# Optimization experiments

Measured on AMD Instinct MI355X. Metric: run time of the kernel, lower is better.

## Reference

```python
import jax, jax.numpy as jnp
import numpy as np

B, N, K = 4, 4096, 16
EPS = 1e-12


def setup_inputs() -> dict:
    key = jax.random.key(0)
    k1, k2, k3 = jax.random.split(key, 3)
    ori = jax.random.normal(k1, (B, N, 3), dtype=jnp.float32)
    # adversarial cloud = original + small perturbation (realistic attack setting)
    adv = ori + 0.05 * jax.random.normal(k2, (B, N, 3), dtype=jnp.float32)
    nrm = jax.random.normal(k3, (B, N, 3), dtype=jnp.float32)
    nrm = nrm / (jnp.linalg.norm(nrm, axis=-1, keepdims=True) + EPS)  # unit normals
    return {"ori_pcs": ori, "adv_pcs": adv, "ori_normals": nrm, "k": K}


def _sqdist(a, b):
    # a: [B,N,3], b: [B,M,3] -> [B,N,M] squared euclidean distances (GEMM form)
    return ((a * a).sum(-1)[:, :, None] + (b * b).sum(-1)[:, None, :]
            - 2.0 * jnp.einsum('bnd,bmd->bnm', a, b))


def _gather_rows(pts, idx):
    # pts: [B,M,3], idx: [B,...] int -> [B,...,3]
    return jax.vmap(lambda p, i: p[i])(pts, idx)


def _kappa(pc, normals, k):
    # curvature proxy: mean |<normalized offset to kNN, normal>| per point -> [B,N]
    d = _sqdist(pc, pc)                       # [B,N,N]
    _, idx = jax.lax.top_k(-d, k + 1)         # nearest k+1 (incl. self)
    idx = idx[..., 1:]                        # drop self -> [B,N,k]
    nn = _gather_rows(pc, idx)                # [B,N,k,3]
    vec = nn - pc[:, :, None, :]
    vec = vec / (jnp.linalg.norm(vec, axis=-1, keepdims=True) + EPS)
    return jnp.abs(jnp.einsum('bnkd,bnd->bnk', vec, normals)).mean(-1)


def reference(ori_pcs, adv_pcs, ori_normals, k):
    # curvature of the clean cloud
    kappa_ori = _kappa(ori_pcs, ori_normals, k)            # [B,N]
    # adv points borrow the normal of their nearest original point
    d = _sqdist(adv_pcs, ori_pcs)                          # [B,N,N]
    nn_idx = jnp.argmin(d, axis=-1)                        # [B,N]
    adv_normals = _gather_rows(ori_normals, nn_idx)        # [B,N,3]
    kappa_adv = _kappa(adv_pcs, adv_normals, k)            # [B,N]
    # std of curvature over points (torch.std -> unbiased, ddof=1)
    std_ori = jnp.std(kappa_ori, axis=1, ddof=1)           # [B]
    std_adv = jnp.std(kappa_adv, axis=1, ddof=1)           # [B]
    return jnp.mean(jnp.abs(std_adv - std_ori))
```

## Files before the change

kernel.cpp:

```cpp
#include <hip/hip_runtime.h>
#include <math.h>

#define B_ 4
#define N_ 4096
#define K_ 16
#define NT 64
#define INF __builtin_huge_valf()
#define SLACK 1e-3f

__device__ __forceinline__ float dpp_shr1_f(float x) {
    return __int_as_float(__builtin_amdgcn_update_dpp(
        __float_as_int(x), __float_as_int(x), 0x111, 0xF, 0xF, false));
}
__device__ __forceinline__ int dpp_shr1_i(int x) {
    return __builtin_amdgcn_update_dpp(x, x, 0x111, 0xF, 0xF, false);
}
__device__ __forceinline__ float readlane_f(float x, int l) {
    return __int_as_float(__builtin_amdgcn_readlane(__float_as_int(x), l));
}
__device__ __forceinline__ float rflf(float x) {
    return __int_as_float(__builtin_amdgcn_readfirstlane(__float_as_int(x)));
}
#if __has_builtin(__builtin_amdgcn_inverse_ballot_w64)
#define LANEBIT(m, lane) __builtin_amdgcn_inverse_ballot_w64(m)
#else
#define LANEBIT(m, lane) ((((m) >> (lane)) & 1ull) != 0)
#endif

#define POP1(mi, di, sdi, sii, tb)                                         \
    {   int src = __builtin_ctzll(mi); mi &= mi - 1;                       \
        float v = readlane_f(di, src);                                     \
        int  vi = (tb) + src;                                              \
        unsigned long long mg = __ballot(sdi > v);                         \
        float usd = dpp_shr1_f(sdi); int usi = dpp_shr1_i(sii);            \
        bool gt = LANEBIT(mg, lane);                                       \
        bool pg = LANEBIT(mg << 1, lane);                                  \
        sdi = gt ? (pg ? usd : v ) : sdi;                                  \
        sii = gt ? (pg ? usi : vi) : sii; }

__device__ __forceinline__ int spread4(int v) {
    return (v & 1) | ((v & 2) << 2) | ((v & 4) << 4) | ((v & 8) << 6);
}

__device__ __forceinline__ float aabb2f(float4 lo, float4 hi,
                                        float qx, float qy, float qz) {
    float dx = fmaxf(fmaxf(lo.x - qx, qx - hi.x), 0.f);
    float dy = fmaxf(fmaxf(lo.y - qy, qy - hi.y), 0.f);
    float dz = fmaxf(fmaxf(lo.z - qz, qz - hi.z), 0.f);
    return fmaf(dz, dz, fmaf(dy, dy, dx*dx));
}

#define TILE_SORT(sk, st)                                                  \
    _Pragma("unroll")                                                      \
    for (int k = 2; k <= 64; k <<= 1) {                                    \
        _Pragma("unroll")                                                  \
        for (int jj = k >> 1; jj > 0; jj >>= 1) {                          \
            bool sel = ((lane & k) == 0) == ((lane & jj) == 0);            \
            float o = __shfl_xor(sk, jj); int a2 = __shfl_xor(st, jj);     \
            bool oless = (o < sk) || (o == sk && a2 < st);                 \
            if (oless == sel) { sk = o; st = a2; }                         \
        }                                                                  \
    }

__global__ __launch_bounds__(1024) void morton_sort_kernel(
    const float* __restrict__ ori, const float* __restrict__ adv,
    float4* __restrict__ gs, int* __restrict__ gidx)
{
    __shared__ int hist[4096];
    __shared__ int wsum[1024];
    const int tid = threadIdx.x;
    const int set = blockIdx.x >> 2, b = blockIdx.x & 3;
    const float* src = (set ? adv : ori) + (size_t)b * (N_*3);
    float4* dst = gs + (size_t)blockIdx.x * N_;
    int*    dsi = gidx + (size_t)blockIdx.x * N_;

    #pragma unroll
    for (int k = 0; k < 4; ++k) hist[k*1024 + tid] = 0;
    __syncthreads();

    float px[4], py[4], pz[4]; int code[4];
    #pragma unroll
    for (int k = 0; k < 4; ++k) {
        int j = k*1024 + tid;
        float x = src[3*j+0], y = src[3*j+1], z = src[3*j+2];
        px[k] = x; py[k] = y; pz[k] = z;
        int ix = (int)((x + 4.25f) * (16.0f/8.5f));
        int iy = (int)((y + 4.25f) * (16.0f/8.5f));
        int iz = (int)((z + 4.25f) * (16.0f/8.5f));
        ix = ix < 0 ? 0 : (ix > 15 ? 15 : ix);
        iy = iy < 0 ? 0 : (iy > 15 ? 15 : iy);
        iz = iz < 0 ? 0 : (iz > 15 ? 15 : iz);
        code[k] = (spread4(ix) << 2) | (spread4(iy) << 1) | spread4(iz);
        atomicAdd(&hist[code[k]], 1);
    }
    __syncthreads();
    const int h0 = hist[4*tid], h1 = hist[4*tid+1],
              h2 = hist[4*tid+2], h3 = hist[4*tid+3];
    const int s = h0 + h1 + h2 + h3;
    wsum[tid] = s;
    __syncthreads();
    for (int st = 1; st < 1024; st <<= 1) {
        int tmp = (tid >= st) ? wsum[tid - st] : 0;
        __syncthreads();
        wsum[tid] += tmp;
        __syncthreads();
    }
    int eb = wsum[tid] - s;
    hist[4*tid]   = eb;
    hist[4*tid+1] = eb + h0;
    hist[4*tid+2] = eb + h0 + h1;
    hist[4*tid+3] = eb + h0 + h1 + h2;
    __syncthreads();
    #pragma unroll
    for (int k = 0; k < 4; ++k) {
        int j = k*1024 + tid;
        int pos = atomicAdd(&hist[code[k]], 1);
        float pp = fmaf(pz[k],pz[k], fmaf(py[k],py[k], px[k]*px[k]));
        dst[pos] = make_float4(px[k], py[k], pz[k], pp);
        dsi[pos] = j;
    }
}

__global__ __launch_bounds__(1024) void aabb_kernel(
    const float4* __restrict__ gs, float4* __restrict__ ab)
{
    const int tid = threadIdx.x, lane = tid & 63, w = tid >> 6;
    const float4* g = gs + (size_t)blockIdx.x * N_;
    float4* a = ab + (size_t)blockIdx.x * (NT*2);
    #pragma unroll
    for (int i = 0; i < 4; ++i) {
        int t = w*4 + i;
        float4 p = g[t*64 + lane];
        float x0=p.x, x1=p.x, y0=p.y, y1=p.y, z0=p.z, z1=p.z;
        #pragma unroll
        for (int s2 = 1; s2 < 64; s2 <<= 1) {
            x0 = fminf(x0, __shfl_xor(x0, s2)); x1 = fmaxf(x1, __shfl_xor(x1, s2));
            y0 = fminf(y0, __shfl_xor(y0, s2)); y1 = fmaxf(y1, __shfl_xor(y1, s2));
            z0 = fminf(z0, __shfl_xor(z0, s2)); z1 = fmaxf(z1, __shfl_xor(z1, s2));
        }
        if (lane == 0) {
            a[t*2+0] = make_float4(x0, y0, z0, 0.f);
            a[t*2+1] = make_float4(x1, y1, z1, 0.f);
        }
    }
}

__global__ __launch_bounds__(256) void curv_argmin_kernel(
    const float4* __restrict__ gs, const int* __restrict__ gidx,
    const float4* __restrict__ ab, int* __restrict__ nnidx)
{
    const int tid = threadIdx.x, lane = tid & 63;
    const int gw = blockIdx.x*4 + (tid >> 6);
    const int b  = gw >> 10;
    const int sq0 = (gw & 1023) * 4;
    const float4* go = gs + (size_t)b * N_;
    const int*    io = gidx + (size_t)b * N_;
    const float4* ga = gs + (size_t)(4+b) * N_;
    const int*    ia = gidx + (size_t)(4+b) * N_;
    const float4* abo = ab + (size_t)b * (NT*2);

    float4 f0 = ga[sq0+0], f1 = ga[sq0+1], f2 = ga[sq0+2], f3 = ga[sq0+3];
    const float q0x=rflf(f0.x), q0y=rflf(f0.y), q0z=rflf(f0.z), qq0=rflf(f0.w);
    const float q1x=rflf(f1.x), q1y=rflf(f1.y), q1z=rflf(f1.z), qq1=rflf(f1.w);
    const float q2x=rflf(f2.x), q2y=rflf(f2.y), q2z=rflf(f2.z), qq2=rflf(f2.w);
    const float q3x=rflf(f3.x), q3y=rflf(f3.y), q3z=rflf(f3.z), qq3=rflf(f3.w);
    const float m2x0=-2.f*q0x, m2y0=-2.f*q0y, m2z0=-2.f*q0z;
    const float m2x1=-2.f*q1x, m2y1=-2.f*q1y, m2z1=-2.f*q1z;
    const float m2x2=-2.f*q2x, m2y2=-2.f*q2y, m2z2=-2.f*q2z;
    const float m2x3=-2.f*q3x, m2y3=-2.f*q3y, m2z3=-2.f*q3z;

    float4 lo = abo[lane*2+0], hi = abo[lane*2+1];
    float sk = fminf(fminf(aabb2f(lo,hi,q0x,q0y,q0z), aabb2f(lo,hi,q1x,q1y,q1z)),
                     fminf(aabb2f(lo,hi,q2x,q2y,q2z), aabb2f(lo,hi,q3x,q3y,q3z)));
    int st = lane;
    TILE_SORT(sk, st)

    float dm0=INF,dm1=INF,dm2=INF,dm3=INF; int jm0=0,jm1=0,jm2=0,jm3=0;
    float bound = INF;
    for (int it = 0; it < NT; ++it) {
        float kd = readlane_f(sk, it);
        if (kd >= bound) break;
        int t = __builtin_amdgcn_readlane(st, it);
        int j = t*64 + lane;
        float4 p = go[j];
        float r0 = fmaf(p.z,m2z0, fmaf(p.y,m2y0, fmaf(p.x,m2x0, p.w)));
        float r1 = fmaf(p.z,m2z1, fmaf(p.y,m2y1, fmaf(p.x,m2x1, p.w)));
        float r2 = fmaf(p.z,m2z2, fmaf(p.y,m2y2, fmaf(p.x,m2x2, p.w)));
        float r3 = fmaf(p.z,m2z3, fmaf(p.y,m2y3, fmaf(p.x,m2x3, p.w)));
        if (r0 < dm0) { dm0 = r0; jm0 = j; }
        if (r1 < dm1) { dm1 = r1; jm1 = j; }
        if (r2 < dm2) { dm2 = r2; jm2 = j; }
        if (r3 < dm3) { dm3 = r3; jm3 = j; }
        float g0=dm0, g1=dm1, g2=dm2, g3=dm3;
        #pragma unroll
        for (int s2 = 1; s2 < 64; s2 <<= 1) {
            g0 = fminf(g0, __shfl_xor(g0, s2));
            g1 = fminf(g1, __shfl_xor(g1, s2));
            g2 = fminf(g2, __shfl_xor(g2, s2));
            g3 = fminf(g3, __shfl_xor(g3, s2));
        }
        bound = fmaxf(fmaxf(g0+qq0, g1+qq1), fmaxf(g2+qq2, g3+qq3)) + SLACK;
    }
    #pragma unroll
    for (int s2 = 1; s2 < 64; s2 <<= 1) {
        { float od=__shfl_xor(dm0,s2); int oj=__shfl_xor(jm0,s2);
          if (od<dm0 || (od==dm0 && oj<jm0)) { dm0=od; jm0=oj; } }
        { float od=__shfl_xor(dm1,s2); int oj=__shfl_xor(jm1,s2);
          if (od<dm1 || (od==dm1 && oj<jm1)) { dm1=od; jm1=oj; } }
        { float od=__shfl_xor(dm2,s2); int oj=__shfl_xor(jm2,s2);
          if (od<dm2 || (od==dm2 && oj<jm2)) { dm2=od; jm2=oj; } }
        { float od=__shfl_xor(dm3,s2); int oj=__shfl_xor(jm3,s2);
          if (od<dm3 || (od==dm3 && oj<jm3)) { dm3=od; jm3=oj; } }
    }
    if (lane == 0) {
        nnidx[b*N_ + ia[sq0+0]] = io[jm0];
        nnidx[b*N_ + ia[sq0+1]] = io[jm1];
        nnidx[b*N_ + ia[sq0+2]] = io[jm2];
        nnidx[b*N_ + ia[sq0+3]] = io[jm3];
    }
}

__global__ __launch_bounds__(256) void curv_kappa_kernel(
    const float4* __restrict__ gs, const int* __restrict__ gidx,
    const float4* __restrict__ ab, const float* __restrict__ nrm,
    const int* __restrict__ nnidx, double* __restrict__ acc)
{
    __shared__ double rs[4], rss[4];
    const int tid = threadIdx.x, lane = tid & 63, w = tid >> 6;
    const int gw = blockIdx.x*4 + w;
    const int job = gw >> 12;
    const int b   = (gw >> 10) & 3;
    const int sq0 = (gw & 1023) * 4;
    const float4* g  = gs + (size_t)(job*4+b) * N_;
    const int*    gi = gidx + (size_t)(job*4+b) * N_;
    const float4* abo = ab + (size_t)(job*4+b) * (NT*2);
    const float*  nb = nrm + (size_t)b * (N_*3);

    const int T0 = sq0 >> 6, sl = sq0 & 63;
    float4 f0 = g[sq0+0], f1 = g[sq0+1], f2 = g[sq0+2], f3 = g[sq0+3];
    const float q0x=rflf(f0.x), q0y=rflf(f0.y), q0z=rflf(f0.z), qq0=rflf(f0.w);
    const float q1x=rflf(f1.x), q1y=rflf(f1.y), q1z=rflf(f1.z), qq1=rflf(f1.w);
    const float q2x=rflf(f2.x), q2y=rflf(f2.y), q2z=rflf(f2.z), qq2=rflf(f2.w);
    const float q3x=rflf(f3.x), q3y=rflf(f3.y), q3z=rflf(f3.z), qq3=rflf(f3.w);
    const float m2x0=-2.f*q0x, m2y0=-2.f*q0y, m2z0=-2.f*q0z;
    const float m2x1=-2.f*q1x, m2y1=-2.f*q1y, m2z1=-2.f*q1z;
    const float m2x2=-2.f*q2x, m2y2=-2.f*q2y, m2z2=-2.f*q2z;
    const float m2x3=-2.f*q3x, m2y3=-2.f*q3y, m2z3=-2.f*q3z;

    const int n0 = __builtin_amdgcn_readfirstlane(gi[sq0+0]);
    const int n1 = __builtin_amdgcn_readfirstlane(gi[sq0+1]);
    const int n2 = __builtin_amdgcn_readfirstlane(gi[sq0+2]);
    const int n3 = __builtin_amdgcn_readfirstlane(gi[sq0+3]);
    const int nn0 = job ? nnidx[b*N_ + n0] : n0;
    const int nn1 = job ? nnidx[b*N_ + n1] : n1;
    const int nn2 = job ? nnidx[b*N_ + n2] : n2;
    const int nn3 = job ? nnidx[b*N_ + n3] : n3;
    const float nx0=rflf(nb[3*nn0+0]), ny0=rflf(nb[3*nn0+1]), nz0=rflf(nb[3*nn0+2]);
    const float nx1=rflf(nb[3*nn1+0]), ny1=rflf(nb[3*nn1+1]), nz1=rflf(nb[3*nn1+2]);
    const float nx2=rflf(nb[3*nn2+0]), ny2=rflf(nb[3*nn2+1]), nz2=rflf(nb[3*nn2+2]);
    const float nx3=rflf(nb[3*nn3+0]), ny3=rflf(nb[3*nn3+1]), nz3=rflf(nb[3*nn3+2]);

    float4 lo = abo[lane*2+0], hi = abo[lane*2+1];
    float sk = fminf(fminf(aabb2f(lo,hi,q0x,q0y,q0z), aabb2f(lo,hi,q1x,q1y,q1z)),
                     fminf(aabb2f(lo,hi,q2x,q2y,q2z), aabb2f(lo,hi,q3x,q3y,q3z)));
    int st = lane;
    TILE_SORT(sk, st)

    const int j0 = T0*64 + lane;
    float sd0, sd1, sd2, sd3;
    int   si0 = j0, si1 = j0, si2 = j0, si3 = j0;
    {
        float4 p = g[j0];
        sd0 = fmaf(p.z,m2z0, fmaf(p.y,m2y0, fmaf(p.x,m2x0, p.w)));
        sd1 = fmaf(p.z,m2z1, fmaf(p.y,m2y1, fmaf(p.x,m2x1, p.w)));
        sd2 = fmaf(p.z,m2z2, fmaf(p.y,m2y2, fmaf(p.x,m2x2, p.w)));
        sd3 = fmaf(p.z,m2z3, fmaf(p.y,m2y3, fmaf(p.x,m2x3, p.w)));
        if (lane == sl    ) sd0 = INF;
        if (lane == sl + 1) sd1 = INF;
        if (lane == sl + 2) sd2 = INF;
        if (lane == sl + 3) sd3 = INF;
    }
    #pragma unroll
    for (int k = 2; k <= 64; k <<= 1) {
        #pragma unroll
        for (int jj = k >> 1; jj > 0; jj >>= 1) {
            bool sel = ((lane & k) == 0) == ((lane & jj) == 0);
            { float o=__shfl_xor(sd0,jj); int a=__shfl_xor(si0,jj);
              if ((o<sd0)==sel) { sd0=o; si0=a; } }
            { float o=__shfl_xor(sd1,jj); int a=__shfl_xor(si1,jj);
              if ((o<sd1)==sel) { sd1=o; si1=a; } }
            { float o=__shfl_xor(sd2,jj); int a=__shfl_xor(si2,jj);
              if ((o<sd2)==sel) { sd2=o; si2=a; } }
            { float o=__shfl_xor(sd3,jj); int a=__shfl_xor(si3,jj);
              if ((o<sd3)==sel) { sd3=o; si3=a; } }
        }
    }
    float tau0 = readlane_f(sd0, 15), tau1 = readlane_f(sd1, 15);
    float tau2 = readlane_f(sd2, 15), tau3 = readlane_f(sd3, 15);
    float bound = fmaxf(fmaxf(tau0+qq0, tau1+qq1),
                        fmaxf(tau2+qq2, tau3+qq3)) + SLACK;

    for (int it = 0; it < NT; ++it) {
        float kd = readlane_f(sk, it);
        if (kd >= bound) break;
        int t = __builtin_amdgcn_readlane(st, it);
        if (t == T0) continue;
        int tb = t*64, j = tb + lane;
        float4 p = g[j];
        float d0 = fmaf(p.z,m2z0, fmaf(p.y,m2y0, fmaf(p.x,m2x0, p.w)));
        float d1 = fmaf(p.z,m2z1, fmaf(p.y,m2y1, fmaf(p.x,m2x1, p.w)));
        float d2 = fmaf(p.z,m2z2, fmaf(p.y,m2y2, fmaf(p.x,m2x2, p.w)));
        float d3 = fmaf(p.z,m2z3, fmaf(p.y,m2y3, fmaf(p.x,m2x3, p.w)));
        unsigned long long m0 = __ballot(d0 < tau0);
        unsigned long long m1 = __ballot(d1 < tau1);
        unsigned long long m2 = __ballot(d2 < tau2);
        unsigned long long m3 = __ballot(d3 < tau3);
        if (m0 | m1 | m2 | m3) {
            while (m0 | m1 | m2 | m3) {
                if (m0) POP1(m0, d0, sd0, si0, tb)
                if (m1) POP1(m1, d1, sd1, si1, tb)
                if (m2) POP1(m2, d2, sd2, si2, tb)
                if (m3) POP1(m3, d3, sd3, si3, tb)
            }
            tau0 = readlane_f(sd0, 15); tau1 = readlane_f(sd1, 15);
            tau2 = readlane_f(sd2, 15); tau3 = readlane_f(sd3, 15);
            bound = fmaxf(fmaxf(tau0+qq0, tau1+qq1),
                          fmaxf(tau2+qq2, tau3+qq3)) + SLACK;
        }
    }

    double ksum = 0.0, kss = 0.0;
#define KTAIL(siN, qxN, qyN, qzN, nxN, nyN, nzN)                           \
    {   float tl = 0.0f;                                                   \
        if (lane < K_) {                                                   \
            float4 p2 = g[siN];                                            \
            float vx = p2.x - qxN, vy = p2.y - qyN, vz = p2.z - qzN;       \
            float L  = sqrtf(vx*vx + vy*vy + vz*vz) + 1e-12f;              \
            tl = fabsf(fmaf(vz,nzN, fmaf(vy,nyN, vx*nxN))) / L;            \
        }                                                                  \
        tl += __shfl_xor(tl, 1); tl += __shfl_xor(tl, 2);                  \
        tl += __shfl_xor(tl, 4); tl += __shfl_xor(tl, 8);                  \
        if (lane == 0) { double kk = (double)tl * (1.0/16.0);              \
                         ksum += kk; kss += kk*kk; } }
    KTAIL(si0, q0x, q0y, q0z, nx0, ny0, nz0)
    KTAIL(si1, q1x, q1y, q1z, nx1, ny1, nz1)
    KTAIL(si2, q2x, q2y, q2z, nx2, ny2, nz2)
    KTAIL(si3, q3x, q3y, q3z, nx3, ny3, nz3)
#undef KTAIL

    if (lane == 0) { rs[w] = ksum; rss[w] = kss; }
    __syncthreads();
    if (tid == 0) {
        double s  = rs[0] + rs[1] + rs[2] + rs[3];
        double ss = rss[0] + rss[1] + rss[2] + rss[3];
        int row = job*4 + b;
        atomicAdd(&acc[row*2+0], s);
        atomicAdd(&acc[row*2+1], ss);
    }
}

__global__ void curv_finalize_kernel(const double* __restrict__ acc,
                                     float* __restrict__ out)
{
    if (threadIdx.x == 0 && blockIdx.x == 0) {
        double st[8];
        #pragma unroll
        for (int r = 0; r < 8; ++r) {
            double s   = acc[2*r+0];
            double ss  = acc[2*r+1];
            double var = (ss - s*s / (double)N_) / (double)(N_ - 1);
            st[r] = var > 0.0 ? sqrt(var) : 0.0;
        }
        double o = 0.0;
        #pragma unroll
        for (int bb = 0; bb < 4; ++bb) o += fabs(st[4+bb] - st[bb]);
        out[0] = (float)(o * 0.25);
    }
}

extern "C" void kernel_launch(void* const* d_in, const int* in_sizes, int n_in,
                              void* d_out, int out_size, void* d_ws, size_t ws_size,
                              hipStream_t stream)
{
    const float* ori = (const float*)d_in[0];
    const float* adv = (const float*)d_in[1];
    const float* nrm = (const float*)d_in[2];
    double* acc   = (double*)d_ws;
    int*    nnidx = (int*)((char*)d_ws + 256);
    float4* gs    = (float4*)((char*)d_ws + 256 + 65536);
    int*    gidx  = (int*)((char*)d_ws + 256 + 65536 + 524288);
    float4* ab    = (float4*)((char*)d_ws + 256 + 65536 + 524288 + 131072);
    float*  out   = (float*)d_out;

    hipMemsetAsync(acc, 0, 16 * sizeof(double), stream);
    morton_sort_kernel<<<8, 1024, 0, stream>>>(ori, adv, gs, gidx);
    aabb_kernel<<<8, 1024, 0, stream>>>(gs, ab);
    curv_argmin_kernel<<<1024, 256, 0, stream>>>(gs, gidx, ab, nnidx);
    curv_kappa_kernel<<<2048, 256, 0, stream>>>(gs, gidx, ab, nrm, nnidx, acc);
    curv_finalize_kernel<<<1, 64, 0, stream>>>(acc, out);
}
```

Baseline: 136.2 us.

## Fuse AABB and argmin into sort/kappa kernels, one query per wave

The AABB computation is folded into the Morton sort kernel, reading the sorted points from shared memory, and the exclusive scan becomes a wave-level shuffle scan instead of a barrier-heavy LDS scan. The separate nearest-normal argmin kernel is dropped; each kappa wave now finds its own nearest original point inline. Each wave handles one query instead of four, so the grid grows from 2048 to 8192 blocks. This removes two launches and the nnidx round trip, and gives each query its own pruning bound instead of a shared worst-case one. The cost is no amortisation of tile loads, sorts and reductions across four queries per wave, plus extra divergence between adv and ori waves.

```diff
diff --git a/kernel.cpp b/kernel.cpp
--- a/kernel.cpp
+++ b/kernel.cpp
@@ -64,15 +64,17 @@
 
 __global__ __launch_bounds__(1024) void morton_sort_kernel(
     const float* __restrict__ ori, const float* __restrict__ adv,
-    float4* __restrict__ gs, int* __restrict__ gidx)
+    float4* __restrict__ gs, int* __restrict__ gidx, float4* __restrict__ ab)
 {
     __shared__ int hist[4096];
-    __shared__ int wsum[1024];
-    const int tid = threadIdx.x;
+    __shared__ int wpart[16];
+    __shared__ float4 spt[N_];
+    const int tid = threadIdx.x, lane = tid & 63, w = tid >> 6;
     const int set = blockIdx.x >> 2, b = blockIdx.x & 3;
     const float* src = (set ? adv : ori) + (size_t)b * (N_*3);
     float4* dst = gs + (size_t)blockIdx.x * N_;
     int*    dsi = gidx + (size_t)blockIdx.x * N_;
+    float4* a   = ab + (size_t)blockIdx.x * (NT*2);
 
     #pragma unroll
     for (int k = 0; k < 4; ++k) hist[k*1024 + tid] = 0;
@@ -97,40 +99,46 @@
     const int h0 = hist[4*tid], h1 = hist[4*tid+1],
               h2 = hist[4*tid+2], h3 = hist[4*tid+3];
     const int s = h0 + h1 + h2 + h3;
-    wsum[tid] = s;
-    __syncthreads();
-    for (int st = 1; st < 1024; st <<= 1) {
-        int tmp = (tid >= st) ? wsum[tid - st] : 0;
-        __syncthreads();
-        wsum[tid] += tmp;
-        __syncthreads();
-    }
-    int eb = wsum[tid] - s;
-    hist[4*tid]   = eb;
-    hist[4*tid+1] = eb + h0;
-    hist[4*tid+2] = eb + h0 + h1;
-    hist[4*tid+3] = eb + h0 + h1 + h2;
+    int inc = s;
+    #pragma unroll
+    for (int d2 = 1; d2 < 64; d2 <<= 1) {
+        int u = __shfl_up(inc, d2);
+        if (lane >= d2) inc += u;
+    }
+    if (lane == 63) wpart[w] = inc;
+    __syncthreads();
+    if (w == 0) {
+        int v = (lane < 16) ? wpart[lane] : 0;
+        int iv = v;
+        #pragma unroll
+        for (int d2 = 1; d2 < 16; d2 <<= 1) {
+            int u = __shfl_up(iv, d2);
+            if (lane >= d2) iv += u;
+        }
+        if (lane < 16) wpart[lane] = iv - v;
+    }
+    __syncthreads();
+    int base = wpart[w] + inc - s;
+    hist[4*tid]   = base;
+    hist[4*tid+1] = base + h0;
+    hist[4*tid+2] = base + h0 + h1;
+    hist[4*tid+3] = base + h0 + h1 + h2;
     __syncthreads();
     #pragma unroll
     for (int k = 0; k < 4; ++k) {
         int j = k*1024 + tid;
         int pos = atomicAdd(&hist[code[k]], 1);
         float pp = fmaf(pz[k],pz[k], fmaf(py[k],py[k], px[k]*px[k]));
-        dst[pos] = make_float4(px[k], py[k], pz[k], pp);
+        float4 f = make_float4(px[k], py[k], pz[k], pp);
+        dst[pos] = f;
+        spt[pos] = f;
         dsi[pos] = j;
     }
-}
-
-__global__ __launch_bounds__(1024) void aabb_kernel(
-    const float4* __restrict__ gs, float4* __restrict__ ab)
-{
-    const int tid = threadIdx.x, lane = tid & 63, w = tid >> 6;
-    const float4* g = gs + (size_t)blockIdx.x * N_;
-    float4* a = ab + (size_t)blockIdx.x * (NT*2);
+    __syncthreads();
     #pragma unroll
     for (int i = 0; i < 4; ++i) {
         int t = w*4 + i;
-        float4 p = g[t*64 + lane];
+        float4 p = spt[t*64 + lane];
         float x0=p.x, x1=p.x, y0=p.y, y1=p.y, z0=p.z, z1=p.z;
         #pragma unroll
         for (int s2 = 1; s2 < 64; s2 <<= 1) {
@@ -145,210 +153,111 @@
     }
 }
 
-__global__ __launch_bounds__(256) void curv_argmin_kernel(
-    const float4* __restrict__ gs, const int* __restrict__ gidx,
-    const float4* __restrict__ ab, int* __restrict__ nnidx)
-{
-    const int tid = threadIdx.x, lane = tid & 63;
-    const int gw = blockIdx.x*4 + (tid >> 6);
-    const int b  = gw >> 10;
-    const int sq0 = (gw & 1023) * 4;
-    const float4* go = gs + (size_t)b * N_;
-    const int*    io = gidx + (size_t)b * N_;
-    const float4* ga = gs + (size_t)(4+b) * N_;
-    const int*    ia = gidx + (size_t)(4+b) * N_;
-    const float4* abo = ab + (size_t)b * (NT*2);
-
-    float4 f0 = ga[sq0+0], f1 = ga[sq0+1], f2 = ga[sq0+2], f3 = ga[sq0+3];
-    const float q0x=rflf(f0.x), q0y=rflf(f0.y), q0z=rflf(f0.z), qq0=rflf(f0.w);
-    const float q1x=rflf(f1.x), q1y=rflf(f1.y), q1z=rflf(f1.z), qq1=rflf(f1.w);
-    const float q2x=rflf(f2.x), q2y=rflf(f2.y), q2z=rflf(f2.z), qq2=rflf(f2.w);
-    const float q3x=rflf(f3.x), q3y=rflf(f3.y), q3z=rflf(f3.z), qq3=rflf(f3.w);
-    const float m2x0=-2.f*q0x, m2y0=-2.f*q0y, m2z0=-2.f*q0z;
-    const float m2x1=-2.f*q1x, m2y1=-2.f*q1y, m2z1=-2.f*q1z;
-    const float m2x2=-2.f*q2x, m2y2=-2.f*q2y, m2z2=-2.f*q2z;
-    const float m2x3=-2.f*q3x, m2y3=-2.f*q3y, m2z3=-2.f*q3z;
-
-    float4 lo = abo[lane*2+0], hi = abo[lane*2+1];
-    float sk = fminf(fminf(aabb2f(lo,hi,q0x,q0y,q0z), aabb2f(lo,hi,q1x,q1y,q1z)),
-                     fminf(aabb2f(lo,hi,q2x,q2y,q2z), aabb2f(lo,hi,q3x,q3y,q3z)));
-    int st = lane;
-    TILE_SORT(sk, st)
-
-    float dm0=INF,dm1=INF,dm2=INF,dm3=INF; int jm0=0,jm1=0,jm2=0,jm3=0;
-    float bound = INF;
-    for (int it = 0; it < NT; ++it) {
-        float kd = readlane_f(sk, it);
-        if (kd >= bound) break;
-        int t = __builtin_amdgcn_readlane(st, it);
-        int j = t*64 + lane;
-        float4 p = go[j];
-        float r0 = fmaf(p.z,m2z0, fmaf(p.y,m2y0, fmaf(p.x,m2x0, p.w)));
-        float r1 = fmaf(p.z,m2z1, fmaf(p.y,m2y1, fmaf(p.x,m2x1, p.w)));
-        float r2 = fmaf(p.z,m2z2, fmaf(p.y,m2y2, fmaf(p.x,m2x2, p.w)));
-        float r3 = fmaf(p.z,m2z3, fmaf(p.y,m2y3, fmaf(p.x,m2x3, p.w)));
-        if (r0 < dm0) { dm0 = r0; jm0 = j; }
-        if (r1 < dm1) { dm1 = r1; jm1 = j; }
-        if (r2 < dm2) { dm2 = r2; jm2 = j; }
-        if (r3 < dm3) { dm3 = r3; jm3 = j; }
-        float g0=dm0, g1=dm1, g2=dm2, g3=dm3;
-        #pragma unroll
-        for (int s2 = 1; s2 < 64; s2 <<= 1) {
-            g0 = fminf(g0, __shfl_xor(g0, s2));
-            g1 = fminf(g1, __shfl_xor(g1, s2));
-            g2 = fminf(g2, __shfl_xor(g2, s2));
-            g3 = fminf(g3, __shfl_xor(g3, s2));
-        }
-        bound = fmaxf(fmaxf(g0+qq0, g1+qq1), fmaxf(g2+qq2, g3+qq3)) + SLACK;
-    }
-    #pragma unroll
-    for (int s2 = 1; s2 < 64; s2 <<= 1) {
-        { float od=__shfl_xor(dm0,s2); int oj=__shfl_xor(jm0,s2);
-          if (od<dm0 || (od==dm0 && oj<jm0)) { dm0=od; jm0=oj; } }
-        { float od=__shfl_xor(dm1,s2); int oj=__shfl_xor(jm1,s2);
-          if (od<dm1 || (od==dm1 && oj<jm1)) { dm1=od; jm1=oj; } }
-        { float od=__shfl_xor(dm2,s2); int oj=__shfl_xor(jm2,s2);
-          if (od<dm2 || (od==dm2 && oj<jm2)) { dm2=od; jm2=oj; } }
-        { float od=__shfl_xor(dm3,s2); int oj=__shfl_xor(jm3,s2);
-          if (od<dm3 || (od==dm3 && oj<jm3)) { dm3=od; jm3=oj; } }
-    }
-    if (lane == 0) {
-        nnidx[b*N_ + ia[sq0+0]] = io[jm0];
-        nnidx[b*N_ + ia[sq0+1]] = io[jm1];
-        nnidx[b*N_ + ia[sq0+2]] = io[jm2];
-        nnidx[b*N_ + ia[sq0+3]] = io[jm3];
-    }
-}
-
 __global__ __launch_bounds__(256) void curv_kappa_kernel(
     const float4* __restrict__ gs, const int* __restrict__ gidx,
     const float4* __restrict__ ab, const float* __restrict__ nrm,
-    const int* __restrict__ nnidx, double* __restrict__ acc)
+    double* __restrict__ acc)
 {
     __shared__ double rs[4], rss[4];
     const int tid = threadIdx.x, lane = tid & 63, w = tid >> 6;
-    const int gw = blockIdx.x*4 + w;
-    const int job = gw >> 12;
-    const int b   = (gw >> 10) & 3;
-    const int sq0 = (gw & 1023) * 4;
+    const int gw  = blockIdx.x*4 + w;
+    const int job = gw >> 14;
+    const int b   = (gw >> 12) & 3;
+    const int sq  = gw & 4095;
     const float4* g  = gs + (size_t)(job*4+b) * N_;
     const int*    gi = gidx + (size_t)(job*4+b) * N_;
     const float4* abo = ab + (size_t)(job*4+b) * (NT*2);
     const float*  nb = nrm + (size_t)b * (N_*3);
 
-    const int T0 = sq0 >> 6, sl = sq0 & 63;
-    float4 f0 = g[sq0+0], f1 = g[sq0+1], f2 = g[sq0+2], f3 = g[sq0+3];
-    const float q0x=rflf(f0.x), q0y=rflf(f0.y), q0z=rflf(f0.z), qq0=rflf(f0.w);
-    const float q1x=rflf(f1.x), q1y=rflf(f1.y), q1z=rflf(f1.z), qq1=rflf(f1.w);
-    const float q2x=rflf(f2.x), q2y=rflf(f2.y), q2z=rflf(f2.z), qq2=rflf(f2.w);
-    const float q3x=rflf(f3.x), q3y=rflf(f3.y), q3z=rflf(f3.z), qq3=rflf(f3.w);
-    const float m2x0=-2.f*q0x, m2y0=-2.f*q0y, m2z0=-2.f*q0z;
-    const float m2x1=-2.f*q1x, m2y1=-2.f*q1y, m2z1=-2.f*q1z;
-    const float m2x2=-2.f*q2x, m2y2=-2.f*q2y, m2z2=-2.f*q2z;
-    const float m2x3=-2.f*q3x, m2y3=-2.f*q3y, m2z3=-2.f*q3z;
-
-    const int n0 = __builtin_amdgcn_readfirstlane(gi[sq0+0]);
-    const int n1 = __builtin_amdgcn_readfirstlane(gi[sq0+1]);
-    const int n2 = __builtin_amdgcn_readfirstlane(gi[sq0+2]);
-    const int n3 = __builtin_amdgcn_readfirstlane(gi[sq0+3]);
-    const int nn0 = job ? nnidx[b*N_ + n0] : n0;
-    const int nn1 = job ? nnidx[b*N_ + n1] : n1;
-    const int nn2 = job ? nnidx[b*N_ + n2] : n2;
-    const int nn3 = job ? nnidx[b*N_ + n3] : n3;
-    const float nx0=rflf(nb[3*nn0+0]), ny0=rflf(nb[3*nn0+1]), nz0=rflf(nb[3*nn0+2]);
-    const float nx1=rflf(nb[3*nn1+0]), ny1=rflf(nb[3*nn1+1]), nz1=rflf(nb[3*nn1+2]);
-    const float nx2=rflf(nb[3*nn2+0]), ny2=rflf(nb[3*nn2+1]), nz2=rflf(nb[3*nn2+2]);
-    const float nx3=rflf(nb[3*nn3+0]), ny3=rflf(nb[3*nn3+1]), nz3=rflf(nb[3*nn3+2]);
+    const int T0 = sq >> 6, sl = sq & 63;
+    float4 f = g[sq];
+    const float qx = rflf(f.x), qy = rflf(f.y), qz = rflf(f.z), qq = rflf(f.w);
+    const float m2x = -2.f*qx, m2y = -2.f*qy, m2z = -2.f*qz;
+
+    float nx, ny, nz;
+    if (job == 0) {
+        int n = __builtin_amdgcn_readfirstlane(gi[sq]);
+        nx = rflf(nb[3*n+0]); ny = rflf(nb[3*n+1]); nz = rflf(nb[3*n+2]);
+    } else {
+        const float4* go  = gs + (size_t)b * N_;
+        const int*    io  = gidx + (size_t)b * N_;
+        const float4* abg = ab + (size_t)b * (NT*2);
+        float4 lo = abg[lane*2+0], hi = abg[lane*2+1];
+        float sk2 = aabb2f(lo, hi, qx, qy, qz); int st2 = lane;
+        TILE_SORT(sk2, st2)
+        float dm = INF; int jm = 0; float bnd = INF;
+        for (int it = 0; it < NT; ++it) {
+            float kd = readlane_f(sk2, it);
+            if (kd >= bnd) break;
+            int t = __builtin_amdgcn_readlane(st2, it);
+            float4 p = go[t*64 + lane];
+            float r = fmaf(p.z,m2z, fmaf(p.y,m2y, fmaf(p.x,m2x, p.w)));
+            if (r < dm) { dm = r; jm = t*64 + lane; }
+            float gm = dm;
+            #pragma unroll
+            for (int s2 = 1; s2 < 64; s2 <<= 1) gm = fminf(gm, __shfl_xor(gm, s2));
+            bnd = gm + qq + SLACK;
+        }
+        #pragma unroll
+        for (int s2 = 1; s2 < 64; s2 <<= 1) {
+            float od = __shfl_xor(dm, s2); int oj = __shfl_xor(jm, s2);
+            if (od < dm || (od == dm && oj < jm)) { dm = od; jm = oj; }
+        }
+        int nn = io[jm];
+        nx = rflf(nb[3*nn+0]); ny = rflf(nb[3*nn+1]); nz = rflf(nb[3*nn+2]);
+    }
 
     float4 lo = abo[lane*2+0], hi = abo[lane*2+1];
-    float sk = fminf(fminf(aabb2f(lo,hi,q0x,q0y,q0z), aabb2f(lo,hi,q1x,q1y,q1z)),
-                     fminf(aabb2f(lo,hi,q2x,q2y,q2z), aabb2f(lo,hi,q3x,q3y,q3z)));
-    int st = lane;
+    float sk = aabb2f(lo, hi, qx, qy, qz); int st = lane;
     TILE_SORT(sk, st)
 
     const int j0 = T0*64 + lane;
-    float sd0, sd1, sd2, sd3;
-    int   si0 = j0, si1 = j0, si2 = j0, si3 = j0;
+    float sd; int si = j0;
     {
         float4 p = g[j0];
-        sd0 = fmaf(p.z,m2z0, fmaf(p.y,m2y0, fmaf(p.x,m2x0, p.w)));
-        sd1 = fmaf(p.z,m2z1, fmaf(p.y,m2y1, fmaf(p.x,m2x1, p.w)));
-        sd2 = fmaf(p.z,m2z2, fmaf(p.y,m2y2, fmaf(p.x,m2x2, p.w)));
-        sd3 = fmaf(p.z,m2z3, fmaf(p.y,m2y3, fmaf(p.x,m2x3, p.w)));
-        if (lane == sl    ) sd0 = INF;
-        if (lane == sl + 1) sd1 = INF;
-        if (lane == sl + 2) sd2 = INF;
-        if (lane == sl + 3) sd3 = INF;
+        sd = fmaf(p.z,m2z, fmaf(p.y,m2y, fmaf(p.x,m2x, p.w)));
+        if (lane == sl) sd = INF;
     }
     #pragma unroll
     for (int k = 2; k <= 64; k <<= 1) {
         #pragma unroll
         for (int jj = k >> 1; jj > 0; jj >>= 1) {
             bool sel = ((lane & k) == 0) == ((lane & jj) == 0);
-            { float o=__shfl_xor(sd0,jj); int a=__shfl_xor(si0,jj);
-              if ((o<sd0)==sel) { sd0=o; si0=a; } }
-            { float o=__shfl_xor(sd1,jj); int a=__shfl_xor(si1,jj);
-              if ((o<sd1)==sel) { sd1=o; si1=a; } }
-            { float o=__shfl_xor(sd2,jj); int a=__shfl_xor(si2,jj);
-              if ((o<sd2)==sel) { sd2=o; si2=a; } }
-            { float o=__shfl_xor(sd3,jj); int a=__shfl_xor(si3,jj);
-              if ((o<sd3)==sel) { sd3=o; si3=a; } }
-        }
-    }
-    float tau0 = readlane_f(sd0, 15), tau1 = readlane_f(sd1, 15);
-    float tau2 = readlane_f(sd2, 15), tau3 = readlane_f(sd3, 15);
-    float bound = fmaxf(fmaxf(tau0+qq0, tau1+qq1),
-                        fmaxf(tau2+qq2, tau3+qq3)) + SLACK;
+            float o = __shfl_xor(sd, jj); int a2 = __shfl_xor(si, jj);
+            if ((o < sd) == sel) { sd = o; si = a2; }
+        }
+    }
+    float tau = readlane_f(sd, 15);
 
     for (int it = 0; it < NT; ++it) {
         float kd = readlane_f(sk, it);
-        if (kd >= bound) break;
+        if (kd >= tau + qq + SLACK) break;
         int t = __builtin_amdgcn_readlane(st, it);
         if (t == T0) continue;
-        int tb = t*64, j = tb + lane;
-        float4 p = g[j];
-        float d0 = fmaf(p.z,m2z0, fmaf(p.y,m2y0, fmaf(p.x,m2x0, p.w)));
-        float d1 = fmaf(p.z,m2z1, fmaf(p.y,m2y1, fmaf(p.x,m2x1, p.w)));
-        float d2 = fmaf(p.z,m2z2, fmaf(p.y,m2y2, fmaf(p.x,m2x2, p.w)));
-        float d3 = fmaf(p.z,m2z3, fmaf(p.y,m2y3, fmaf(p.x,m2x3, p.w)));
-        unsigned long long m0 = __ballot(d0 < tau0);
-        unsigned long long m1 = __ballot(d1 < tau1);
-        unsigned long long m2 = __ballot(d2 < tau2);
-        unsigned long long m3 = __ballot(d3 < tau3);
-        if (m0 | m1 | m2 | m3) {
-            while (m0 | m1 | m2 | m3) {
-                if (m0) POP1(m0, d0, sd0, si0, tb)
-                if (m1) POP1(m1, d1, sd1, si1, tb)
-                if (m2) POP1(m2, d2, sd2, si2, tb)
-                if (m3) POP1(m3, d3, sd3, si3, tb)
-            }
-            tau0 = readlane_f(sd0, 15); tau1 = readlane_f(sd1, 15);
-            tau2 = readlane_f(sd2, 15); tau3 = readlane_f(sd3, 15);
-            bound = fmaxf(fmaxf(tau0+qq0, tau1+qq1),
-                          fmaxf(tau2+qq2, tau3+qq3)) + SLACK;
-        }
-    }
-
-    double ksum = 0.0, kss = 0.0;
-#define KTAIL(siN, qxN, qyN, qzN, nxN, nyN, nzN)                           \
-    {   float tl = 0.0f;                                                   \
-        if (lane < K_) {                                                   \
-            float4 p2 = g[siN];                                            \
-            float vx = p2.x - qxN, vy = p2.y - qyN, vz = p2.z - qzN;       \
-            float L  = sqrtf(vx*vx + vy*vy + vz*vz) + 1e-12f;              \
-            tl = fabsf(fmaf(vz,nzN, fmaf(vy,nyN, vx*nxN))) / L;            \
-        }                                                                  \
-        tl += __shfl_xor(tl, 1); tl += __shfl_xor(tl, 2);                  \
-        tl += __shfl_xor(tl, 4); tl += __shfl_xor(tl, 8);                  \
-        if (lane == 0) { double kk = (double)tl * (1.0/16.0);              \
-                         ksum += kk; kss += kk*kk; } }
-    KTAIL(si0, q0x, q0y, q0z, nx0, ny0, nz0)
-    KTAIL(si1, q1x, q1y, q1z, nx1, ny1, nz1)
-    KTAIL(si2, q2x, q2y, q2z, nx2, ny2, nz2)
-    KTAIL(si3, q3x, q3y, q3z, nx3, ny3, nz3)
-#undef KTAIL
-
-    if (lane == 0) { rs[w] = ksum; rss[w] = kss; }
+        int tb = t*64;
+        float4 p = g[tb + lane];
+        float d = fmaf(p.z,m2z, fmaf(p.y,m2y, fmaf(p.x,m2x, p.w)));
+        unsigned long long m = __ballot(d < tau);
+        if (m) {
+            do { POP1(m, d, sd, si, tb) } while (m);
+            tau = readlane_f(sd, 15);
+        }
+    }
+
+    float tl = 0.0f;
+    if (lane < K_) {
+        float4 p2 = g[si];
+        float vx = p2.x - qx, vy = p2.y - qy, vz = p2.z - qz;
+        float L  = sqrtf(vx*vx + vy*vy + vz*vz) + 1e-12f;
+        tl = fabsf(fmaf(vz,nz, fmaf(vy,ny, vx*nx))) / L;
+    }
+    tl += __shfl_xor(tl, 1); tl += __shfl_xor(tl, 2);
+    tl += __shfl_xor(tl, 4); tl += __shfl_xor(tl, 8);
+
+    if (lane == 0) {
+        double kap = (double)tl * (1.0/16.0);
+        rs[w] = kap; rss[w] = kap*kap;
+    }
     __syncthreads();
     if (tid == 0) {
         double s  = rs[0] + rs[1] + rs[2] + rs[3];
@@ -385,17 +294,14 @@
     const float* ori = (const float*)d_in[0];
     const float* adv = (const float*)d_in[1];
     const float* nrm = (const float*)d_in[2];
-    double* acc   = (double*)d_ws;
-    int*    nnidx = (int*)((char*)d_ws + 256);
-    float4* gs    = (float4*)((char*)d_ws + 256 + 65536);
-    int*    gidx  = (int*)((char*)d_ws + 256 + 65536 + 524288);
-    float4* ab    = (float4*)((char*)d_ws + 256 + 65536 + 524288 + 131072);
-    float*  out   = (float*)d_out;
+    double* acc  = (double*)d_ws;
+    float4* gs   = (float4*)((char*)d_ws + 256);
+    int*    gidx = (int*)((char*)d_ws + 256 + 524288);
+    float4* ab   = (float4*)((char*)d_ws + 256 + 524288 + 131072);
+    float*  out  = (float*)d_out;
 
     hipMemsetAsync(acc, 0, 16 * sizeof(double), stream);
-    morton_sort_kernel<<<8, 1024, 0, stream>>>(ori, adv, gs, gidx);
-    aabb_kernel<<<8, 1024, 0, stream>>>(gs, ab);
-    curv_argmin_kernel<<<1024, 256, 0, stream>>>(gs, gidx, ab, nnidx);
-    curv_kappa_kernel<<<2048, 256, 0, stream>>>(gs, gidx, ab, nrm, nnidx, acc);
+    morton_sort_kernel<<<8, 1024, 0, stream>>>(ori, adv, gs, gidx, ab);
+    curv_kappa_kernel<<<8192, 256, 0, stream>>>(gs, gidx, ab, nrm, acc);
     curv_finalize_kernel<<<1, 64, 0, stream>>>(acc, out);
 }
```

Result: slower. 198.1 us (+45.4%).
